# Kernel tuning notes

Measured on AMD Instinct MI355X. Metric: run time of the kernel, lower is better.

Reference implementation:

```python
import jax, jax.numpy as jnp
import numpy as np

B, N, D, H = 16384, 64, 64, 128
DECAY_W = 2.0  # Decayer(2, 'rev') -> 1 / (1 + w * dt)
EPS = 1e-12


def setup_inputs() -> dict:
    key = jax.random.key(0)
    ks = jax.random.split(key, 16)
    return {
        "dt_node": jax.random.uniform(ks[0], (B,)) * 10.0,
        "deg_node": jax.random.uniform(ks[1], (B,)),
        "cc_node": jax.random.uniform(ks[2], (B,)),
        "dt_neigh": jax.random.uniform(ks[3], (B, N)) * 10.0,
        "deg_neigh": jax.random.uniform(ks[4], (B, N)),
        "cc_neigh": jax.random.uniform(ks[5], (B, N)),
        "neigh_mask": jax.random.bernoulli(ks[6], 0.7, (B, N)),
        "feature_hist": jax.random.normal(ks[7], (B, 2 * D)),
        "t2v_w": jax.random.normal(ks[8], (D,)) * 0.1,
        "t2v_b": jax.random.normal(ks[9], (D,)) * 0.1,
        "node_w": jax.random.normal(ks[10], (D,)) * 0.1,
        "node_b": jax.random.normal(ks[11], (D,)) * 0.1,
        "att_W1": jax.random.normal(ks[12], (D, D)) * (1.0 / np.sqrt(D)),
        "att_W2": jax.random.normal(ks[13], (D, D)) * (1.0 / np.sqrt(D)),
        "att_v": jax.random.normal(ks[14], (D,)) * (1.0 / np.sqrt(D)),
        "weight": jax.random.normal(ks[15], (H, 4 * D)) * (1.0 / np.sqrt(4 * D)),
    }


def _time2vec(t, w, b):
    # Time2Vec('cos'): first channel linear, rest cos-activated. t: [...], -> [..., D]
    v = t[..., None] * w + b
    return jnp.concatenate([v[..., :1], jnp.cos(v[..., 1:])], axis=-1)


def _node_feat(dt, deg, cc, t2v_w, t2v_b, node_w, node_b):
    # linear_node(deg) + linear_node(cc) + time2vec(|dt|), then L2 normalize
    f = (_time2vec(jnp.abs(dt), t2v_w, t2v_b)
         + (deg[..., None] * node_w + node_b)
         + (cc[..., None] * node_w + node_b))
    nrm = jnp.maximum(jnp.linalg.norm(f, axis=-1, keepdims=True), EPS)
    return f / nrm


def reference(dt_node, deg_node, cc_node, dt_neigh, deg_neigh, cc_neigh,
              neigh_mask, feature_hist, t2v_w, t2v_b, node_w, node_b,
              att_W1, att_W2, att_v, weight):
    node_f = _node_feat(dt_node, deg_node, cc_node, t2v_w, t2v_b, node_w, node_b)      # [B, D]
    neigh_f = _node_feat(dt_neigh, deg_neigh, cc_neigh, t2v_w, t2v_b, node_w, node_b)  # [B, N, D]

    # temporal decay: Decayer(2, 'rev')
    time_score = 1.0 / (1.0 + DECAY_W * dt_neigh)                                       # [B, N]

    h = jnp.tanh((node_f @ att_W1)[:, None, :] + jnp.einsum('bnd,de->bne', neigh_f, att_W2))
    att = jnp.einsum('bne,e->bn', h, att_v)                                             # [B, N]

    score = jax.nn.leaky_relu(time_score) * att                                         # [B, N]
    m = neigh_mask.astype(node_f.dtype)
    n_in = jnp.maximum(jnp.sum(m, axis=-1, keepdims=True), 1.0)                         # [B, 1]
    w_n = (m * score) / n_in                                                            # [B, N]
    neigh_agg = jnp.einsum('bn,bnd->bd', w_n, neigh_f)                                  # [B, D]

    combined = jnp.concatenate([node_f, neigh_agg, feature_hist], axis=-1)              # [B, 4D]
    return jax.nn.relu(combined @ weight.T)                                             # [B, H]
```

## Files before the change

### kernel.cpp

```cpp
#include <hip/hip_runtime.h>
#include <hip/hip_bf16.h>

#define B_SZ 16384
#define N_SZ 64
#define D_SZ 64
#define H_SZ 128
#define R_PB 4
#define ARS 68
#define CRS 264

typedef short bf16x8 __attribute__((ext_vector_type(8)));
typedef float f32x4  __attribute__((ext_vector_type(4)));

__device__ __forceinline__ float bflo(unsigned u){union{unsigned i;float f;}c;c.i=u<<16;return c.f;}
__device__ __forceinline__ float bfhi(unsigned u){union{unsigned i;float f;}c;c.i=u&0xffff0000u;return c.f;}
__device__ __forceinline__ float bits2f(unsigned short r){union{unsigned i;float f;}c;c.i=((unsigned)r)<<16;return c.f;}
__device__ __forceinline__ unsigned f2bfbits(float f){
    __hip_bfloat16 h = __float2bfloat16(f);
    unsigned short u;
    __builtin_memcpy(&u, &h, 2);
    return (unsigned)u;
}
__device__ __forceinline__ unsigned pack2bf(float a, float b){
    __hip_bfloat162 h = __float22bfloat162_rn(make_float2(a, b));
    unsigned r;
    __builtin_memcpy(&r, &h, 4);
    return r;
}
__device__ __forceinline__ float bf2f(__hip_bfloat16 x) { return __bfloat162float(x); }

template<int CTRL>
__device__ __forceinline__ float dpp_add(float v){
    int t = __builtin_amdgcn_mov_dpp(__builtin_bit_cast(int, v), CTRL, 0xf, 0xf, true);
    return v + __builtin_bit_cast(float, t);
}

__device__ __forceinline__ float tanh_fast(float x){
    float e = __expf(2.0f * x);
    return 1.0f - __fdividef(2.0f, e + 1.0f);
}

template<int FMODE>
__device__ __forceinline__ float LD(const void* p, int i) {
    if constexpr (FMODE == 0) return bf2f(((const __hip_bfloat16*)p)[i]);
    else                      return ((const float*)p)[i];
}

template<int FMODE>
__device__ __forceinline__ void load16(const void* p, int off, float* o) {
    if constexpr (FMODE == 0) {
        const uint4* q = (const uint4*)((const unsigned short*)p + off);
        uint4 a = q[0], b = q[1];
        o[0]=bflo(a.x); o[1]=bfhi(a.x); o[2]=bflo(a.y); o[3]=bfhi(a.y);
        o[4]=bflo(a.z); o[5]=bfhi(a.z); o[6]=bflo(a.w); o[7]=bfhi(a.w);
        o[8]=bflo(b.x); o[9]=bfhi(b.x); o[10]=bflo(b.y); o[11]=bfhi(b.y);
        o[12]=bflo(b.z); o[13]=bfhi(b.z); o[14]=bflo(b.w); o[15]=bfhi(b.w);
    } else {
        const float4* q = (const float4*)((const float*)p + off);
        float4 a=q[0],b=q[1],c=q[2],d=q[3];
        o[0]=a.x;o[1]=a.y;o[2]=a.z;o[3]=a.w; o[4]=b.x;o[5]=b.y;o[6]=b.z;o[7]=b.w;
        o[8]=c.x;o[9]=c.y;o[10]=c.z;o[11]=c.w; o[12]=d.x;o[13]=d.y;o[14]=d.z;o[15]=d.w;
    }
}

__device__ __forceinline__ float mval(const void* p, int i, int mode) {
    if (mode == 0) return ((const int*)p)[i]            ? 1.0f : 0.0f;
    if (mode == 1) return ((const unsigned char*)p)[i]  ? 1.0f : 0.0f;
    if (mode == 2) return ((const unsigned short*)p)[i] ? 1.0f : 0.0f;
    return ((const unsigned int*)p)[i]                  ? 1.0f : 0.0f;
}

__device__ __forceinline__ int detect_f32(const void* p) {
    const uint4* q = (const uint4*)p;
    unsigned o = 0;
    #pragma unroll
    for (int i = 0; i < 8; ++i) { uint4 v = q[i]; o |= v.x | v.y | v.z | v.w; }
    return (o & 0x80008000u) ? 1 : 0;
}

__device__ __forceinline__ int detect_mask_mode(const void* p) {
    const uint4* q = (const uint4*)p;
    unsigned oa = 0, ofe = 0;
    #pragma unroll
    for (int i = 0; i < 8; ++i) {
        uint4 v = q[i];
        unsigned w = v.x | v.y | v.z | v.w;
        oa  |= w;
        ofe |= (v.x & 0xFEFEFEFEu) | (v.y & 0xFEFEFEFEu) | (v.z & 0xFEFEFEFEu) | (v.w & 0xFEFEFEFEu);
    }
    if ((oa & 0xFFFFFF00u) == 0) return 0;
    if (ofe == 0)                return 1;
    if (oa & 0x000000FEu)        return 2;
    return 3;
}

__global__ void prep_kernel(const void* dt_node, const void* att_W1, const void* att_W2,
                            void* ws) {
    const int t     = blockIdx.x * 256 + threadIdx.x;
    const int fmode = detect_f32(dt_node);
    const int fi  = t >> 6, ln = t & 63;
    const int et  = fi >> 2, ks = fi & 3;
    const int m16 = ln & 15, qd = ln >> 4;
    const int col = et * 16 + m16;
    unsigned short s[8];
    #pragma unroll
    for (int j = 0; j < 8; ++j) {
        const int i = ks * 32 + qd * 8 + j;
        if (fmode == 0) {
            s[j] = (i < 64) ? ((const unsigned short*)att_W1)[i * D_SZ + col]
                            : ((const unsigned short*)att_W2)[(i - 64) * D_SZ + col];
        } else {
            const float v = (i < 64) ? ((const float*)att_W1)[i * D_SZ + col]
                                     : ((const float*)att_W2)[(i - 64) * D_SZ + col];
            s[j] = (unsigned short)f2bfbits(v);
        }
    }
    ((uint4*)ws)[t] = make_uint4(((unsigned)s[0]) | (((unsigned)s[1]) << 16),
                                 ((unsigned)s[2]) | (((unsigned)s[3]) << 16),
                                 ((unsigned)s[4]) | (((unsigned)s[5]) << 16),
                                 ((unsigned)s[6]) | (((unsigned)s[7]) << 16));
}

struct Smem {
    alignas(16) unsigned short A[R_PB * 65 * ARS];
    alignas(16) unsigned short comb[R_PB * CRS];
    float att[R_PB][N_SZ];
    float wn[R_PB][N_SZ];
};

template<int FMODE>
__device__ __forceinline__ void feat_row(float t, float dc,
                                         const float* w16, const float* b16_,
                                         const float* nw16, const float* nb16,
                                         int c, unsigned short* dstA, unsigned short* dstC) {
    float f[16]; float ss = 0.0f;
    #pragma unroll
    for (int j = 0; j < 16; ++j) {
        float v  = fmaf(t, w16[j], b16_[j]);
        float tv = (c == 0 && j == 0) ? v : __cosf(v);
        f[j] = tv + fmaf(dc, nw16[j], nb16[j]);
        ss = fmaf(f[j], f[j], ss);
    }
    ss += __shfl_xor(ss, 1, 4);
    ss += __shfl_xor(ss, 2, 4);
    const float inv = 1.0f / fmaxf(sqrtf(ss), 1e-12f);
    unsigned pk[8];
    #pragma unroll
    for (int j = 0; j < 8; ++j)
        pk[j] = pack2bf(f[2*j] * inv, f[2*j+1] * inv);
    uint4 v0 = make_uint4(pk[0], pk[1], pk[2], pk[3]);
    uint4 v1 = make_uint4(pk[4], pk[5], pk[6], pk[7]);
    ((uint4*)dstA)[0] = v0; ((uint4*)dstA)[1] = v1;
    if (dstC) { ((uint4*)dstC)[0] = v0; ((uint4*)dstC)[1] = v1; }
}

template<int FMODE, bool USE_WS>
__device__ __forceinline__ void body(
    Smem& sm,
    const void* dt_node, const void* deg_node, const void* cc_node,
    const void* dt_neigh, const void* deg_neigh, const void* cc_neigh,
    const void* neigh_mask, const void* feature_hist,
    const void* t2v_w, const void* t2v_b, const void* node_w, const void* node_b,
    const void* att_W1, const void* att_W2, const void* att_v,
    const void* weight, void* out, const void* ws, int mmode, int b0, int tid)
{
    const int lane = tid & 63;
    const int wv   = tid >> 6;
    const int m16  = lane & 15;
    const int quad = lane >> 4;

    {
        const int c = tid & 3, d0 = c * 16;
        float w16[16], b16_[16], nw16[16], nb16[16];
        load16<FMODE>(t2v_w,  d0, w16);
        load16<FMODE>(t2v_b,  d0, b16_);
        load16<FMODE>(node_w, d0, nw16);
        load16<FMODE>(node_b, d0, nb16);
        #pragma unroll
        for (int j = 0; j < 16; ++j) nb16[j] *= 2.0f;

        #pragma unroll
        for (int it = 0; it < 5; ++it) {
            const int t = tid + it * 256;
            if (t < R_PB * 65 * 4) {
                const int f = t >> 2;
                if (f < R_PB * 64) {
                    const int row = f >> 6, n = f & 63;
                    const int idx = (b0 + row) * N_SZ + n;
                    const float tn  = fabsf(LD<FMODE>(dt_neigh, idx));
                    const float dcn = LD<FMODE>(deg_neigh, idx) + LD<FMODE>(cc_neigh, idx);
                    feat_row<FMODE>(tn, dcn, w16, b16_, nw16, nb16, c,
                                    sm.A + (row * 65 + n) * ARS + d0, nullptr);
                } else {
                    const int row = f - R_PB * 64;
                    const float tn = fabsf(LD<FMODE>(dt_node, b0 + row));
                    const float dc = LD<FMODE>(deg_node, b0 + row) + LD<FMODE>(cc_node, b0 + row);
                    feat_row<FMODE>(tn, dc, w16, b16_, nw16, nb16, c,
                                    sm.A + (row * 65 + 64) * ARS + d0,
                                    sm.comb + row * CRS + d0);
                }
            }
        }
    }
    __syncthreads();

    {
        const int r = wv;
        const unsigned short* An = sm.A + (r * 65 + 64) * ARS + quad * 8;
        const bf16x8 a0 = *(const bf16x8*)An;
        const bf16x8 a1 = *(const bf16x8*)(An + 32);
        const bf16x8* wfrag = (const bf16x8*)ws;

        f32x4  accN[4];
        bf16x8 w2f[4], w3f[4];
        float  ve[4];
        #pragma unroll
        for (int et = 0; et < 4; ++et) {
            bf16x8 w0, w1;
            if constexpr (USE_WS) {
                w0      = wfrag[(et * 4 + 0) * 64 + lane];
                w1      = wfrag[(et * 4 + 1) * 64 + lane];
                w2f[et] = wfrag[(et * 4 + 2) * 64 + lane];
                w3f[et] = wfrag[(et * 4 + 3) * 64 + lane];
            } else {
                const int col = et * 16 + m16;
                #pragma unroll
                for (int j = 0; j < 8; ++j) {
                    const int k0 = quad * 8 + j;
                    if constexpr (FMODE == 0) {
                        w0[j]      = (short)((const unsigned short*)att_W1)[k0 * D_SZ + col];
                        w1[j]      = (short)((const unsigned short*)att_W1)[(k0 + 32) * D_SZ + col];
                        w2f[et][j] = (short)((const unsigned short*)att_W2)[k0 * D_SZ + col];
                        w3f[et][j] = (short)((const unsigned short*)att_W2)[(k0 + 32) * D_SZ + col];
                    } else {
                        w0[j]      = (short)f2bfbits(((const float*)att_W1)[k0 * D_SZ + col]);
                        w1[j]      = (short)f2bfbits(((const float*)att_W1)[(k0 + 32) * D_SZ + col]);
                        w2f[et][j] = (short)f2bfbits(((const float*)att_W2)[k0 * D_SZ + col]);
                        w3f[et][j] = (short)f2bfbits(((const float*)att_W2)[(k0 + 32) * D_SZ + col]);
                    }
                }
            }
            f32x4 z = {0.f, 0.f, 0.f, 0.f};
            z = __builtin_amdgcn_mfma_f32_16x16x32_bf16(a0, w0, z, 0, 0, 0);
            z = __builtin_amdgcn_mfma_f32_16x16x32_bf16(a1, w1, z, 0, 0, 0);
            accN[et] = z;
            ve[et]   = LD<FMODE>(att_v, et * 16 + m16);
        }

        #pragma unroll
        for (int mt = 0; mt < 4; ++mt) {
            const unsigned short* Ar = sm.A + (r * 65 + mt * 16 + m16) * ARS + quad * 8;
            const bf16x8 a2 = *(const bf16x8*)Ar;
            const bf16x8 a3 = *(const bf16x8*)(Ar + 32);
            float p0 = 0.f, p1 = 0.f, p2 = 0.f, p3 = 0.f;
            #pragma unroll
            for (int et = 0; et < 4; ++et) {
                f32x4 acc = __builtin_amdgcn_mfma_f32_16x16x32_bf16(a2, w2f[et], accN[et], 0, 0, 0);
                acc       = __builtin_amdgcn_mfma_f32_16x16x32_bf16(a3, w3f[et], acc,      0, 0, 0);
                p0 = fmaf(tanh_fast(acc[0]), ve[et], p0);
                p1 = fmaf(tanh_fast(acc[1]), ve[et], p1);
                p2 = fmaf(tanh_fast(acc[2]), ve[et], p2);
                p3 = fmaf(tanh_fast(acc[3]), ve[et], p3);
            }
            p0 = dpp_add<0xB1>(p0); p0 = dpp_add<0x4E>(p0); p0 = dpp_add<0x124>(p0); p0 = dpp_add<0x128>(p0);
            p1 = dpp_add<0xB1>(p1); p1 = dpp_add<0x4E>(p1); p1 = dpp_add<0x124>(p1); p1 = dpp_add<0x128>(p1);
            p2 = dpp_add<0xB1>(p2); p2 = dpp_add<0x4E>(p2); p2 = dpp_add<0x124>(p2); p2 = dpp_add<0x128>(p2);
            p3 = dpp_add<0xB1>(p3); p3 = dpp_add<0x4E>(p3); p3 = dpp_add<0x124>(p3); p3 = dpp_add<0x128>(p3);
            if (m16 == 0) {
                sm.att[r][mt * 16 + quad * 4 + 0] = p0;
                sm.att[r][mt * 16 + quad * 4 + 1] = p1;
                sm.att[r][mt * 16 + quad * 4 + 2] = p2;
                sm.att[r][mt * 16 + quad * 4 + 3] = p3;
            }
        }
    }

    {
        const int r   = wv;
        const int idx = (b0 + r) * N_SZ + lane;
        const float dt = LD<FMODE>(dt_neigh, idx);
        const float ts = 1.0f / fmaf(2.0f, dt, 1.0f);
        const float lr = ts >= 0.0f ? ts : 0.01f * ts;
        const float m  = mval(neigh_mask, idx, mmode);
        float cnt = m;
        #pragma unroll
        for (int off = 32; off > 0; off >>= 1) cnt += __shfl_down(cnt, off, 64);
        cnt = __shfl(cnt, 0, 64);
        sm.wn[r][lane] = m * lr * sm.att[r][lane] / fmaxf(cnt, 1.0f);

        if constexpr (FMODE == 0) {
            const unsigned u = ((const unsigned*)feature_hist)[(b0 + r) * 64 + lane];
            *(unsigned*)(sm.comb + r * CRS + 2 * D_SZ + 2 * lane) = u;
        } else {
            const float* fh = (const float*)feature_hist + (b0 + r) * 2 * D_SZ + 2 * lane;
            *(unsigned*)(sm.comb + r * CRS + 2 * D_SZ + 2 * lane) = pack2bf(fh[0], fh[1]);
        }
    }

    {
        const int r = wv;
        float agg = 0.0f;
        #pragma unroll
        for (int n = 0; n < N_SZ; ++n) {
            const float w = sm.wn[r][n];
            agg = fmaf(w, bits2f(sm.A[(r * 65 + n) * ARS + lane]), agg);
        }
        sm.comb[r * CRS + D_SZ + lane] = (unsigned short)f2bfbits(agg);
    }
    __syncthreads();

    {
        #pragma unroll
        for (int t2 = 0; t2 < 2; ++t2) {
            const int nt = wv * 2 + t2;
            f32x4 c = {0.f, 0.f, 0.f, 0.f};
            #pragma unroll
            for (int ks = 0; ks < 8; ++ks) {
                const bf16x8 af = *(const bf16x8*)(sm.comb + (m16 & 3) * CRS + ks * 32 + quad * 8);
                bf16x8 bw;
                if constexpr (FMODE == 0) {
                    bw = *(const bf16x8*)((const unsigned short*)weight
                            + (nt * 16 + m16) * (4 * D_SZ) + ks * 32 + quad * 8);
                } else {
                    const float* wr = (const float*)weight
                            + (nt * 16 + m16) * (4 * D_SZ) + ks * 32 + quad * 8;
                    #pragma unroll
                    for (int j = 0; j < 8; ++j) bw[j] = (short)f2bfbits(wr[j]);
                }
                c = __builtin_amdgcn_mfma_f32_16x16x32_bf16(af, bw, c, 0, 0, 0);
            }
            if (quad == 0) {
                #pragma unroll
                for (int rr = 0; rr < 4; ++rr) {
                    const float v = fmaxf(c[rr], 0.0f);
                    if constexpr (FMODE == 0)
                        ((__hip_bfloat16*)out)[(b0 + rr) * H_SZ + nt * 16 + m16] = __float2bfloat16(v);
                    else
                        ((float*)out)[(b0 + rr) * H_SZ + nt * 16 + m16] = v;
                }
            }
        }
    }
}

template<bool USE_WS>
__global__ __launch_bounds__(256, 4) void fused_model_kernel(
    const void* dt_node, const void* deg_node, const void* cc_node,
    const void* dt_neigh, const void* deg_neigh, const void* cc_neigh,
    const void* neigh_mask, const void* feature_hist,
    const void* t2v_w, const void* t2v_b, const void* node_w, const void* node_b,
    const void* att_W1, const void* att_W2, const void* att_v,
    const void* weight, void* out, const void* ws)
{
    __shared__ Smem sm;
    const int b0  = blockIdx.x * R_PB;
    const int tid = threadIdx.x;

    const int fmode = __builtin_amdgcn_readfirstlane(detect_f32(dt_node));
    const int mmode = __builtin_amdgcn_readfirstlane(detect_mask_mode(neigh_mask));

    if (fmode == 0)
        body<0, USE_WS>(sm, dt_node, deg_node, cc_node, dt_neigh, deg_neigh, cc_neigh,
                        neigh_mask, feature_hist, t2v_w, t2v_b, node_w, node_b,
                        att_W1, att_W2, att_v, weight, out, ws, mmode, b0, tid);
    else
        body<1, USE_WS>(sm, dt_node, deg_node, cc_node, dt_neigh, deg_neigh, cc_neigh,
                        neigh_mask, feature_hist, t2v_w, t2v_b, node_w, node_b,
                        att_W1, att_W2, att_v, weight, out, ws, mmode, b0, tid);
}

extern "C" void kernel_launch(void* const* d_in, const int* in_sizes, int n_in,
                              void* d_out, int out_size, void* d_ws, size_t ws_size,
                              hipStream_t stream) {
    const bool use_ws = (ws_size >= 16384) && (d_ws != nullptr);
    if (use_ws) {
        prep_kernel<<<4, 256, 0, stream>>>(d_in[0], d_in[12], d_in[13], d_ws);
        fused_model_kernel<true><<<B_SZ / R_PB, 256, 0, stream>>>(
            d_in[0], d_in[1], d_in[2], d_in[3], d_in[4], d_in[5], d_in[6], d_in[7],
            d_in[8], d_in[9], d_in[10], d_in[11], d_in[12], d_in[13], d_in[14], d_in[15],
            d_out, d_ws);
    } else {
        fused_model_kernel<false><<<B_SZ / R_PB, 256, 0, stream>>>(
            d_in[0], d_in[1], d_in[2], d_in[3], d_in[4], d_in[5], d_in[6], d_in[7],
            d_in[8], d_in[9], d_in[10], d_in[11], d_in[12], d_in[13], d_in[14], d_in[15],
            d_out, d_ws);
    }
}
```

Baseline: 218.5 us.

## Halve rows per block and split attention work across wave pairs

```diff
diff --git a/kernel.cpp b/kernel.cpp
--- a/kernel.cpp
+++ b/kernel.cpp
@@ -5,7 +5,7 @@
 #define N_SZ 64
 #define D_SZ 64
 #define H_SZ 128
-#define R_PB 4
+#define R_PB 2
 #define ARS 68
 #define CRS 264
 
@@ -180,7 +180,7 @@
         for (int j = 0; j < 16; ++j) nb16[j] *= 2.0f;
 
         #pragma unroll
-        for (int it = 0; it < 5; ++it) {
+        for (int it = 0; it < 3; ++it) {
             const int t = tid + it * 256;
             if (t < R_PB * 65 * 4) {
                 const int f = t >> 2;
@@ -205,77 +205,73 @@
     __syncthreads();
 
     {
-        const int r = wv;
+        const int r      = wv >> 1;
+        const int mtbase = (wv & 1) * 2;
         const unsigned short* An = sm.A + (r * 65 + 64) * ARS + quad * 8;
         const bf16x8 a0 = *(const bf16x8*)An;
         const bf16x8 a1 = *(const bf16x8*)(An + 32);
         const bf16x8* wfrag = (const bf16x8*)ws;
 
-        f32x4  accN[4];
-        bf16x8 w2f[4], w3f[4];
-        float  ve[4];
+        float p[2][4] = {{0.f,0.f,0.f,0.f},{0.f,0.f,0.f,0.f}};
         #pragma unroll
         for (int et = 0; et < 4; ++et) {
-            bf16x8 w0, w1;
+            bf16x8 w0, w1, w2, w3;
             if constexpr (USE_WS) {
-                w0      = wfrag[(et * 4 + 0) * 64 + lane];
-                w1      = wfrag[(et * 4 + 1) * 64 + lane];
-                w2f[et] = wfrag[(et * 4 + 2) * 64 + lane];
-                w3f[et] = wfrag[(et * 4 + 3) * 64 + lane];
+                w0 = wfrag[(et * 4 + 0) * 64 + lane];
+                w1 = wfrag[(et * 4 + 1) * 64 + lane];
+                w2 = wfrag[(et * 4 + 2) * 64 + lane];
+                w3 = wfrag[(et * 4 + 3) * 64 + lane];
             } else {
                 const int col = et * 16 + m16;
                 #pragma unroll
                 for (int j = 0; j < 8; ++j) {
                     const int k0 = quad * 8 + j;
                     if constexpr (FMODE == 0) {
-                        w0[j]      = (short)((const unsigned short*)att_W1)[k0 * D_SZ + col];
-                        w1[j]      = (short)((const unsigned short*)att_W1)[(k0 + 32) * D_SZ + col];
-                        w2f[et][j] = (short)((const unsigned short*)att_W2)[k0 * D_SZ + col];
-                        w3f[et][j] = (short)((const unsigned short*)att_W2)[(k0 + 32) * D_SZ + col];
+                        w0[j] = (short)((const unsigned short*)att_W1)[k0 * D_SZ + col];
+                        w1[j] = (short)((const unsigned short*)att_W1)[(k0 + 32) * D_SZ + col];
+                        w2[j] = (short)((const unsigned short*)att_W2)[k0 * D_SZ + col];
+                        w3[j] = (short)((const unsigned short*)att_W2)[(k0 + 32) * D_SZ + col];
                     } else {
-                        w0[j]      = (short)f2bfbits(((const float*)att_W1)[k0 * D_SZ + col]);
-                        w1[j]      = (short)f2bfbits(((const float*)att_W1)[(k0 + 32) * D_SZ + col]);
-                        w2f[et][j] = (short)f2bfbits(((const float*)att_W2)[k0 * D_SZ + col]);
-                        w3f[et][j] = (short)f2bfbits(((const float*)att_W2)[(k0 + 32) * D_SZ + col]);
+                        w0[j] = (short)f2bfbits(((const float*)att_W1)[k0 * D_SZ + col]);
+                        w1[j] = (short)f2bfbits(((const float*)att_W1)[(k0 + 32) * D_SZ + col]);
+                        w2[j] = (short)f2bfbits(((const float*)att_W2)[k0 * D_SZ + col]);
+                        w3[j] = (short)f2bfbits(((const float*)att_W2)[(k0 + 32) * D_SZ + col]);
                     }
                 }
             }
             f32x4 z = {0.f, 0.f, 0.f, 0.f};
             z = __builtin_amdgcn_mfma_f32_16x16x32_bf16(a0, w0, z, 0, 0, 0);
             z = __builtin_amdgcn_mfma_f32_16x16x32_bf16(a1, w1, z, 0, 0, 0);
-            accN[et] = z;
-            ve[et]   = LD<FMODE>(att_v, et * 16 + m16);
-        }
-
-        #pragma unroll
-        for (int mt = 0; mt < 4; ++mt) {
-            const unsigned short* Ar = sm.A + (r * 65 + mt * 16 + m16) * ARS + quad * 8;
-            const bf16x8 a2 = *(const bf16x8*)Ar;
-            const bf16x8 a3 = *(const bf16x8*)(Ar + 32);
-            float p0 = 0.f, p1 = 0.f, p2 = 0.f, p3 = 0.f;
+            const float ve = LD<FMODE>(att_v, et * 16 + m16);
             #pragma unroll
-            for (int et = 0; et < 4; ++et) {
-                f32x4 acc = __builtin_amdgcn_mfma_f32_16x16x32_bf16(a2, w2f[et], accN[et], 0, 0, 0);
-                acc       = __builtin_amdgcn_mfma_f32_16x16x32_bf16(a3, w3f[et], acc,      0, 0, 0);
-                p0 = fmaf(tanh_fast(acc[0]), ve[et], p0);
-                p1 = fmaf(tanh_fast(acc[1]), ve[et], p1);
-                p2 = fmaf(tanh_fast(acc[2]), ve[et], p2);
-                p3 = fmaf(tanh_fast(acc[3]), ve[et], p3);
-            }
-            p0 = dpp_add<0xB1>(p0); p0 = dpp_add<0x4E>(p0); p0 = dpp_add<0x124>(p0); p0 = dpp_add<0x128>(p0);
-            p1 = dpp_add<0xB1>(p1); p1 = dpp_add<0x4E>(p1); p1 = dpp_add<0x124>(p1); p1 = dpp_add<0x128>(p1);
-            p2 = dpp_add<0xB1>(p2); p2 = dpp_add<0x4E>(p2); p2 = dpp_add<0x124>(p2); p2 = dpp_add<0x128>(p2);
-            p3 = dpp_add<0xB1>(p3); p3 = dpp_add<0x4E>(p3); p3 = dpp_add<0x124>(p3); p3 = dpp_add<0x128>(p3);
-            if (m16 == 0) {
-                sm.att[r][mt * 16 + quad * 4 + 0] = p0;
-                sm.att[r][mt * 16 + quad * 4 + 1] = p1;
-                sm.att[r][mt * 16 + quad * 4 + 2] = p2;
-                sm.att[r][mt * 16 + quad * 4 + 3] = p3;
-            }
-        }
-    }
-
-    {
+            for (int mi = 0; mi < 2; ++mi) {
+                const unsigned short* Ar = sm.A + (r * 65 + (mtbase + mi) * 16 + m16) * ARS + quad * 8;
+                const bf16x8 a2 = *(const bf16x8*)Ar;
+                const bf16x8 a3 = *(const bf16x8*)(Ar + 32);
+                f32x4 acc = __builtin_amdgcn_mfma_f32_16x16x32_bf16(a2, w2, z,   0, 0, 0);
+                acc       = __builtin_amdgcn_mfma_f32_16x16x32_bf16(a3, w3, acc, 0, 0, 0);
+                p[mi][0] = fmaf(tanh_fast(acc[0]), ve, p[mi][0]);
+                p[mi][1] = fmaf(tanh_fast(acc[1]), ve, p[mi][1]);
+                p[mi][2] = fmaf(tanh_fast(acc[2]), ve, p[mi][2]);
+                p[mi][3] = fmaf(tanh_fast(acc[3]), ve, p[mi][3]);
+            }
+        }
+        #pragma unroll
+        for (int mi = 0; mi < 2; ++mi) {
+            #pragma unroll
+            for (int rr = 0; rr < 4; ++rr) {
+                float s = p[mi][rr];
+                s = dpp_add<0xB1>(s);
+                s = dpp_add<0x4E>(s);
+                s = dpp_add<0x124>(s);
+                s = dpp_add<0x128>(s);
+                if (m16 == 0) sm.att[r][(mtbase + mi) * 16 + quad * 4 + rr] = s;
+            }
+        }
+    }
+    __syncthreads();
+
+    if (wv < R_PB) {
         const int r   = wv;
         const int idx = (b0 + r) * N_SZ + lane;
         const float dt = LD<FMODE>(dt_neigh, idx);
@@ -288,6 +284,15 @@
         cnt = __shfl(cnt, 0, 64);
         sm.wn[r][lane] = m * lr * sm.att[r][lane] / fmaxf(cnt, 1.0f);
 
+        float agg = 0.0f;
+        #pragma unroll
+        for (int n = 0; n < N_SZ; ++n) {
+            const float w = sm.wn[r][n];
+            agg = fmaf(w, bits2f(sm.A[(r * 65 + n) * ARS + lane]), agg);
+        }
+        sm.comb[r * CRS + D_SZ + lane] = (unsigned short)f2bfbits(agg);
+    } else {
+        const int r = wv - R_PB;
         if constexpr (FMODE == 0) {
             const unsigned u = ((const unsigned*)feature_hist)[(b0 + r) * 64 + lane];
             *(unsigned*)(sm.comb + r * CRS + 2 * D_SZ + 2 * lane) = u;
@@ -296,17 +301,6 @@
             *(unsigned*)(sm.comb + r * CRS + 2 * D_SZ + 2 * lane) = pack2bf(fh[0], fh[1]);
         }
     }
-
-    {
-        const int r = wv;
-        float agg = 0.0f;
-        #pragma unroll
-        for (int n = 0; n < N_SZ; ++n) {
-            const float w = sm.wn[r][n];
-            agg = fmaf(w, bits2f(sm.A[(r * 65 + n) * ARS + lane]), agg);
-        }
-        sm.comb[r * CRS + D_SZ + lane] = (unsigned short)f2bfbits(agg);
-    }
     __syncthreads();
 
     {
@@ -316,7 +310,7 @@
             f32x4 c = {0.f, 0.f, 0.f, 0.f};
             #pragma unroll
             for (int ks = 0; ks < 8; ++ks) {
-                const bf16x8 af = *(const bf16x8*)(sm.comb + (m16 & 3) * CRS + ks * 32 + quad * 8);
+                const bf16x8 af = *(const bf16x8*)(sm.comb + (m16 & 1) * CRS + ks * 32 + quad * 8);
                 bf16x8 bw;
                 if constexpr (FMODE == 0) {
                     bw = *(const bf16x8*)((const unsigned short*)weight
@@ -331,7 +325,7 @@
             }
             if (quad == 0) {
                 #pragma unroll
-                for (int rr = 0; rr < 4; ++rr) {
+                for (int rr = 0; rr < R_PB; ++rr) {
                     const float v = fmaxf(c[rr], 0.0f);
                     if constexpr (FMODE == 0)
                         ((__hip_bfloat16*)out)[(b0 + rr) * H_SZ + nt * 16 + m16] = __float2bfloat16(v);
@@ -344,7 +338,7 @@
 }
 
 template<bool USE_WS>
-__global__ __launch_bounds__(256, 4) void fused_model_kernel(
+__global__ __launch_bounds__(256, 8) void fused_model_kernel(
     const void* dt_node, const void* deg_node, const void* cc_node,
     const void* dt_neigh, const void* deg_neigh, const void* cc_neigh,
     const void* neigh_mask, const void* feature_hist,
```

New measurement: 473.8 us. 2.17x slower.
